# Kernel optimization log

Measured on AMD Instinct MI355X. Metric: run time of the kernel, lower is better.

The kernel has to match this reference:

```python
import jax, jax.numpy as jnp
import numpy as np

LUMINANCE_Q = np.array([
    [16, 11, 10, 16, 24, 40, 51, 61],
    [12, 12, 14, 19, 26, 58, 60, 55],
    [14, 13, 16, 24, 40, 57, 69, 56],
    [14, 17, 22, 29, 51, 87, 80, 62],
    [18, 22, 37, 56, 68, 109, 103, 77],
    [24, 36, 55, 64, 81, 104, 113, 92],
    [49, 64, 78, 87, 103, 121, 120, 101],
    [72, 92, 95, 98, 112, 100, 103, 99]], dtype=np.float64) / 100.0

def _dct_matrix():
    # C[k, n] = grid_factors[k] * cos(pi*k*(2n+1)/16); grid_factors = 2*[1/sqrt(32), 1/sqrt(16)x7]
    k = np.arange(8)[:, None]
    n = np.arange(8)[None, :]
    a = np.full(8, 2.0 / np.sqrt(2 * 8))
    a[0] = 2.0 / np.sqrt(4 * 8)
    C = a[:, None] * np.cos(np.pi * k * (2 * n + 1) / 16.0)
    return jnp.asarray(C, dtype=jnp.float32)

DCT_C = _dct_matrix()
Q_TABLE = jnp.asarray(LUMINANCE_Q, dtype=jnp.float32)

def setup_inputs() -> dict:
    key = jax.random.key(0)
    k1, k2 = jax.random.split(key)
    B, H, W = 16, 1024, 1024
    # pixel-like values around 128
    image = 128.0 + 40.0 * jax.random.normal(k1, (B, 1, H, W), dtype=jnp.float32)
    quality_factor = jax.random.randint(k2, (B,), 1, 100).astype(jnp.float32)
    return {"image": image, "quality_factor": quality_factor}

def reference(image, quality_factor):
    B, _, H, W = image.shape
    # Set_QF: factor per batch element, shape [B,1,1,1,1]
    factor = jnp.where(quality_factor < 50.0,
                       5000.0 / quality_factor,
                       200.0 - 2.0 * quality_factor).reshape(B, 1, 1, 1, 1)
    # Image_2_Blocks: [B, H/8, 8, W/8, 8] -> [B, 8, 8, H/8, W/8], then center
    blocks = image.reshape(B, H // 8, 8, W // 8, 8).transpose(0, 2, 4, 1, 3) - 128.0
    # 2D orthonormal DCT-II over the two 8-wide in-block axes (axes 1 then 2)
    dct = jnp.einsum('un,vm,bnmij->buvij', DCT_C, DCT_C, blocks)
    out = dct / (factor * Q_TABLE[None, :, :, None, None])
    # quantize=False: no rounding
    return out.reshape(B, 64, H // 8, W // 8)
```

## Files before the change

kernel.cpp:

```cpp
#include <hip/hip_runtime.h>
#include <cstddef>


static constexpr double LUMQ[64] = {
    16, 11, 10, 16, 24, 40, 51, 61,
    12, 12, 14, 19, 26, 58, 60, 55,
    14, 13, 16, 24, 40, 57, 69, 56,
    14, 17, 22, 29, 51, 87, 80, 62,
    18, 22, 37, 56, 68, 109, 103, 77,
    24, 36, 55, 64, 81, 104, 113, 92,
    49, 64, 78, 87, 103, 121, 120, 101,
    72, 92, 95, 98, 112, 100, 103, 99,
};

static constexpr double AANS[8] = {
    1.0, 1.3870398453221475, 1.3065629648763766, 1.1758756024193588,
    1.0, 0.7856949583871022, 0.5411961001461970, 0.2758993792829430,
};

__device__ __host__ __forceinline__ constexpr float outScale(int u, int v) {
    return (float)(100.0 / (LUMQ[u * 8 + v] * 8.0 * AANS[u] * AANS[v]));
}

__device__ __forceinline__ void aan_dct8(float& x0, float& x1, float& x2,
                                         float& x3, float& x4, float& x5,
                                         float& x6, float& x7) {
    const float t0 = x0 + x7, t7 = x0 - x7;
    const float t1 = x1 + x6, t6 = x1 - x6;
    const float t2 = x2 + x5, t5 = x2 - x5;
    const float t3 = x3 + x4, t4 = x3 - x4;

    float t10 = t0 + t3;
    const float t13 = t0 - t3;
    const float t11 = t1 + t2;
    const float t12 = t1 - t2;
    x0 = t10 + t11;
    x4 = t10 - t11;
    const float z1 = (t12 + t13) * 0.70710678118654752f;
    x2 = t13 + z1;
    x6 = t13 - z1;

    t10 = t4 + t5;
    const float u11 = t5 + t6;
    const float u12 = t6 + t7;
    const float z5 = (t10 - u12) * 0.38268343236508977f;
    const float z2 = 0.54119610014619698f * t10 + z5;
    const float z4 = 1.30656296487637653f * u12 + z5;
    const float z3 = u11 * 0.70710678118654752f;
    const float z11 = t7 + z3;
    const float z13 = t7 - z3;
    x5 = z13 + z2;
    x3 = z13 - z2;
    x1 = z11 + z4;
    x7 = z11 - z4;
}

__global__ __launch_bounds__(256) void jpeg_dct_quant_kernel(
    const float* __restrict__ img,
    const float* __restrict__ qfv,
    float* __restrict__ out)
{
    __shared__ float lds[32 * 256];

    const int tid = threadIdx.x;
    const int wg = blockIdx.x;
    const int bid = wg * 256 + tid;
    const int j = bid & 127;
    const int irow = bid >> 7;
    const int b = bid >> 14;

    const float* src = img + ((size_t)b << 20)
                     + (size_t)((irow & 127) * 8) * 1024 + j * 8;

    float m[8][8];
    #pragma unroll
    for (int n = 0; n < 8; ++n) {
        const float4 r0 = *reinterpret_cast<const float4*>(src + (size_t)n * 1024);
        const float4 r1 = *reinterpret_cast<const float4*>(src + (size_t)n * 1024 + 4);
        m[n][0] = r0.x; m[n][1] = r0.y; m[n][2] = r0.z; m[n][3] = r0.w;
        m[n][4] = r1.x; m[n][5] = r1.y; m[n][6] = r1.z; m[n][7] = r1.w;
    }

    #pragma unroll
    for (int n = 0; n < 8; ++n)
        aan_dct8(m[n][0], m[n][1], m[n][2], m[n][3],
                 m[n][4], m[n][5], m[n][6], m[n][7]);

    #pragma unroll
    for (int v = 0; v < 8; ++v)
        aan_dct8(m[0][v], m[1][v], m[2][v], m[3][v],
                 m[4][v], m[5][v], m[6][v], m[7][v]);

    m[0][0] -= 8192.0f;

    const float qf = qfv[b];
    const float factor = (qf < 50.0f) ? (5000.0f / qf) : (200.0f - 2.0f * qf);
    const float invf = 1.0f / factor;

    #pragma unroll
    for (int u = 0; u < 8; ++u)
        #pragma unroll
        for (int v = 0; v < 8; ++v)
            m[u][v] *= invf * outScale(u, v);

    const int a  = tid >> 7;
    const int w  = tid >> 6;
    const int l  = tid & 63;
    const int i0 = (wg << 1) & 127;

    float* dstbase = out + ((size_t)b << 20) + (size_t)i0 * 128 + (l << 2);

    #pragma unroll
    for (int phase = 0; phase < 2; ++phase) {
        if (phase) __syncthreads();

        #pragma unroll
        for (int u = phase * 4; u < phase * 4 + 4; ++u)
            #pragma unroll
            for (int v = 0; v < 8; ++v)
                lds[(u * 8 + v - phase * 32) * 256 + a * 128 + j] = m[u][v];
        __syncthreads();

        #pragma unroll
        for (int k = 0; k < 8; ++k) {
            const int cl = w * 8 + k;
            const int c  = phase * 32 + cl;
            *reinterpret_cast<float4*>(dstbase + (size_t)c * 16384) =
                *reinterpret_cast<const float4*>(&lds[cl * 256 + (l << 2)]);
        }
    }
}

extern "C" void kernel_launch(void* const* d_in, const int* in_sizes, int n_in,
                              void* d_out, int out_size, void* d_ws, size_t ws_size,
                              hipStream_t stream) {
    const float* img = (const float*)d_in[0];
    const float* qfv = (const float*)d_in[1];
    float* out = (float*)d_out;

    jpeg_dct_quant_kernel<<<1024, 256, 0, stream>>>(img, qfv, out);
}
```

Measured before the change: 112.0 us.

## Stage input strips through swizzled LDS for coalesced global loads

Each workgroup now loads two full 8-row image strips with fully coalesced float4 loads into LDS, using an XOR swizzle to avoid bank conflicts. Each thread then gathers its 8x8 block from LDS instead of issuing strided per-thread global loads. The aim is better global-memory coalescing on the read side. In exchange it adds extra barriers and serializes the two strip loads, which limits memory-level parallelism, and half the threads sit idle during each gather.

```diff
diff --git a/kernel.cpp b/kernel.cpp
--- a/kernel.cpp
+++ b/kernel.cpp
@@ -55,31 +55,58 @@
     x7 = z11 - z4;
 }
 
+__device__ __forceinline__ void stage_strip(const float* __restrict__ strip,
+                                            float* __restrict__ lds, int tid) {
+    float4 r[8];
+    #pragma unroll
+    for (int q = 0; q < 8; ++q)
+        r[q] = *reinterpret_cast<const float4*>(strip + (size_t)((q << 8) + tid) * 4);
+    const int phys = tid ^ ((tid >> 1) & 7);
+    #pragma unroll
+    for (int q = 0; q < 8; ++q)
+        *reinterpret_cast<float4*>(lds + (q << 10) + (phys << 2)) = r[q];
+}
+
+__device__ __forceinline__ void gather_block(const float* __restrict__ lds,
+                                             int jcol, float m[8][8]) {
+    const int p0 = (2 * jcol) ^ (jcol & 7);
+    #pragma unroll
+    for (int n = 0; n < 8; ++n) {
+        const float4 lo = *reinterpret_cast<const float4*>(lds + (n << 10) + (p0 << 2));
+        const float4 hi = *reinterpret_cast<const float4*>(lds + (n << 10) + ((p0 ^ 1) << 2));
+        m[n][0] = lo.x; m[n][1] = lo.y; m[n][2] = lo.z; m[n][3] = lo.w;
+        m[n][4] = hi.x; m[n][5] = hi.y; m[n][6] = hi.z; m[n][7] = hi.w;
+    }
+}
+
 __global__ __launch_bounds__(256) void jpeg_dct_quant_kernel(
     const float* __restrict__ img,
     const float* __restrict__ qfv,
     float* __restrict__ out)
 {
-    __shared__ float lds[32 * 256];
+    __shared__ float lds[8192];
 
     const int tid = threadIdx.x;
-    const int wg = blockIdx.x;
-    const int bid = wg * 256 + tid;
-    const int j = bid & 127;
-    const int irow = bid >> 7;
-    const int b = bid >> 14;
+    const int wg  = blockIdx.x;
+    const int a   = tid >> 7;
+    const int j   = tid & 127;
+    const int R0  = wg << 1;
+    const int b   = R0 >> 7;
+    const int i0  = R0 & 127;
 
-    const float* src = img + ((size_t)b << 20)
-                     + (size_t)((irow & 127) * 8) * 1024 + j * 8;
+    const float* stripA = img + ((size_t)b << 20) + (size_t)i0 * 8192;
+    const float* stripB = stripA + 8192;
 
     float m[8][8];
-    #pragma unroll
-    for (int n = 0; n < 8; ++n) {
-        const float4 r0 = *reinterpret_cast<const float4*>(src + (size_t)n * 1024);
-        const float4 r1 = *reinterpret_cast<const float4*>(src + (size_t)n * 1024 + 4);
-        m[n][0] = r0.x; m[n][1] = r0.y; m[n][2] = r0.z; m[n][3] = r0.w;
-        m[n][4] = r1.x; m[n][5] = r1.y; m[n][6] = r1.z; m[n][7] = r1.w;
-    }
+
+    stage_strip(stripA, lds, tid);
+    __syncthreads();
+    if (a == 0) gather_block(lds, j, m);
+    __syncthreads();
+
+    stage_strip(stripB, lds, tid);
+    __syncthreads();
+    if (a == 1) gather_block(lds, j, m);
 
     #pragma unroll
     for (int n = 0; n < 8; ++n)
@@ -103,16 +130,13 @@
         for (int v = 0; v < 8; ++v)
             m[u][v] *= invf * outScale(u, v);
 
-    const int a  = tid >> 7;
-    const int w  = tid >> 6;
-    const int l  = tid & 63;
-    const int i0 = (wg << 1) & 127;
-
+    const int w = tid >> 6;
+    const int l = tid & 63;
     float* dstbase = out + ((size_t)b << 20) + (size_t)i0 * 128 + (l << 2);
 
     #pragma unroll
     for (int phase = 0; phase < 2; ++phase) {
-        if (phase) __syncthreads();
+        __syncthreads();
 
         #pragma unroll
         for (int u = phase * 4; u < phase * 4 + 4; ++u)
```

Measured after the change: 112.2 us. About the same (+0.2%).
